# Kernel optimization log

Hardware: AMD Instinct MI355X
Metric: run time of the kernel (lower is better)

## Reference

```python
import jax, jax.numpy as jnp
import numpy as np

COORD_W, EDGE_W, COUNT_W, REG_W, CONTRA_W = 1.0, 2.0, 0.1, 0.001, 0.1
MARGIN = 1.0


def setup_inputs() -> dict:
    key = jax.random.key(0)
    ks = jax.random.split(key, 6)
    B, N, D, C = 16, 1024, 128, 2
    return {
        "predicted_coords": jax.random.normal(ks[0], (B, N, C), jnp.float32),
        "points": jax.random.normal(ks[1], (B, N, C), jnp.float32),
        "adjacency_logits": jax.random.normal(ks[2], (B, N, N), jnp.float32),
        "adjacency": jax.random.bernoulli(ks[3], 0.1, (B, N, N)).astype(jnp.float32),
        "node_masks": jnp.ones((B, N), jnp.float32),  # all nodes valid -> n_actual = N
        "predicted_count": jax.random.normal(ks[4], (B, 1), jnp.float32),
        "node_features": jax.random.normal(ks[5], (B, N, D), jnp.float32),
    }


def _bce_with_logits(logits, targets):
    # mean-reduced, numerically stable (matches F.binary_cross_entropy_with_logits)
    return jnp.mean(jnp.maximum(logits, 0.0) - logits * targets
                    + jnp.log1p(jnp.exp(-jnp.abs(logits))))


def _smooth_l1(pred, target):
    d = jnp.abs(pred - target)
    return jnp.mean(jnp.where(d < 1.0, 0.5 * d * d, d - 0.5))


def _contrastive_sample(features, adj):
    # features: [N, D], adj: [N, N]. torch.cdist pairwise euclidean via gram trick.
    nrm = jnp.sum(features * features, axis=-1)              # [N]
    sq = jnp.maximum(nrm[:, None] + nrm[None, :]
                     - 2.0 * (features @ features.T), 0.0)   # [N, N] squared dists
    n = features.shape[0]
    eye = jnp.eye(n, dtype=bool)
    pos_mask = adj > 0.5
    neg_mask = (adj <= 0.5) & (~eye)
    # positive term: mean of distances**2 over positive pairs == mean squared dist
    pos = jnp.sum(jnp.where(pos_mask, sq, 0.0)) / jnp.maximum(jnp.sum(pos_mask), 1)
    dist = jnp.sqrt(jnp.maximum(sq, 1e-12))
    hinge = jnp.square(jax.nn.relu(MARGIN - dist))
    neg = jnp.sum(jnp.where(neg_mask, hinge, 0.0)) / jnp.maximum(jnp.sum(neg_mask), 1)
    return pos + neg


def reference(predicted_coords, points, adjacency_logits, adjacency,
              node_masks, predicted_count, node_features):
    # node_masks are all ones, so the per-sample [:n_actual] slicing is the
    # full tensor; per-sample MSE/BCE means averaged over batch equal global means.
    coord_loss = jnp.mean(jnp.square(predicted_coords - points))
    edge_loss = _bce_with_logits(adjacency_logits, adjacency)
    actual_counts = jnp.sum(node_masks, axis=1)              # [B]
    count_loss = _smooth_l1(predicted_count[:, 0], actual_counts)
    reg_loss = jnp.mean(jnp.square(node_features))
    # contrastive path uses targets['adjacency'] (no predicted_adjacency key)
    contra_loss = jnp.mean(jax.vmap(_contrastive_sample)(node_features, adjacency))
    total = (COORD_W * coord_loss + EDGE_W * edge_loss + COUNT_W * count_loss
             + REG_W * reg_loss + CONTRA_W * contra_loss)
    return total, coord_loss, edge_loss, count_loss, reg_loss, contra_loss
```

## Files before the change

kernel.cpp:

```cpp
#include <hip/hip_runtime.h>
#include <hip/hip_bf16.h>

#define NN    1024
#define DD    128
#define TILE  128
#define PITCH 136
#define SQP   132
#define NBLK  1024

typedef __bf16 bf16_t;
typedef bf16_t bf16x8 __attribute__((ext_vector_type(8)));
typedef float  f32x4  __attribute__((ext_vector_type(4)));


__global__ __launch_bounds__(256) void small_losses(
    const float* __restrict__ pcoord, const float* __restrict__ pts,
    const float* __restrict__ masks,  const float* __restrict__ pcount,
    float* __restrict__ ws) {
  __shared__ float sh[4][2];
  float coord = 0.f, cnt = 0.f;

  const int gt = blockIdx.x * 256 + threadIdx.x;
  const int stride = 16 * 256;

  const float4* a4 = (const float4*)pcoord;
  const float4* b4 = (const float4*)pts;
  for (int i = gt; i < 8192; i += stride) {
    float4 a = a4[i], b = b4[i];
    float dx = a.x-b.x, dy = a.y-b.y, dz = a.z-b.z, dw = a.w-b.w;
    coord += dx*dx + dy*dy + dz*dz + dw*dw;
  }
  const float* m = masks + blockIdx.x * NN;
  for (int i = threadIdx.x; i < NN; i += 256) cnt += m[i];

  const int lane = threadIdx.x & 63, w = threadIdx.x >> 6;
  #pragma unroll
  for (int o = 32; o; o >>= 1) {
    coord += __shfl_xor(coord, o);
    cnt   += __shfl_xor(cnt, o);
  }
  if (lane == 0) { sh[w][0] = coord; sh[w][1] = cnt; }
  __syncthreads();
  if (threadIdx.x == 0) {
    float c = 0.f, n = 0.f;
    for (int i = 0; i < 4; ++i) { c += sh[i][0]; n += sh[i][1]; }
    atomicAdd(&ws[0], c);
    float d = fabsf(pcount[blockIdx.x] - n);
    float term = (d < 1.f) ? 0.5f * d * d : d - 0.5f;
    atomicAdd(&ws[2], term);
  }
}

__device__ __forceinline__ void loss_elem(float l, float a, float s, int grow, int gcol,
    float& bsum, float& poss, float& posc, float& negs, float& negc) {
  bsum += fmaxf(l, 0.f) - l * a + __logf(1.f + __expf(-fabsf(l)));
  if (a > 0.5f) {
    poss += s; posc += 1.f;
  } else if (grow != gcol) {
    negc += 1.f;
    if (s < 1.f) {
      float d = sqrtf(fmaxf(s, 1e-12f));
      float h = 1.f - d;
      negs += h * h;
    }
  }
}

__global__ __launch_bounds__(512, 4) void fused_gram_bce(
    const float* __restrict__ logits, const float* __restrict__ adj,
    const float* __restrict__ feat, float* __restrict__ ws) {
  __shared__ __align__(16) char smem[2 * TILE * PITCH * sizeof(bf16_t)];
  bf16_t* lsA = (bf16_t*)smem;
  bf16_t* lsB = (bf16_t*)(smem + TILE * PITCH * sizeof(bf16_t));
  float*  sqb = (float*)smem;
  __shared__ float nrmA[TILE], nrmB[TILE];
  __shared__ float red[8][6];

  const int bx  = blockIdx.x;
  const int b   = bx >> 6;
  const int tid = bx & 63;
  const int ti  = (tid >> 3) << 7;
  const int tj  = (tid & 7)  << 7;
  const bool diag = ((tid >> 3) == (tid & 7));

  const int t = threadIdx.x;
  const float* fb = feat + (size_t)b * NN * DD;

  float regsum = 0.f;
  #pragma unroll
  for (int it = 0; it < 8; ++it) {
    int cid  = it * 512 + t;
    int tile = cid >> 11;
    int sub  = cid & 2047;
    int row  = sub >> 4;
    int c8   = sub & 15;
    const float* src = fb + (size_t)((tile ? tj : ti) + row) * DD + c8 * 8;
    float4 u = *(const float4*)src;
    float4 v = *(const float4*)(src + 4);
    if (diag && tile == 0)
      regsum += u.x*u.x + u.y*u.y + u.z*u.z + u.w*u.w
              + v.x*v.x + v.y*v.y + v.z*v.z + v.w*v.w;
    bf16_t* dst = (tile ? lsB : lsA) + row * PITCH + c8 * 8;
    dst[0] = (bf16_t)u.x; dst[1] = (bf16_t)u.y; dst[2] = (bf16_t)u.z; dst[3] = (bf16_t)u.w;
    dst[4] = (bf16_t)v.x; dst[5] = (bf16_t)v.y; dst[6] = (bf16_t)v.z; dst[7] = (bf16_t)v.w;
  }
  __syncthreads();

  {
    int row  = t >> 1;
    int half = t & 1;
    const bf16_t* src = (row < TILE ? lsA + row * PITCH : lsB + (row - TILE) * PITCH)
                        + half * 64;
    float s = 0.f;
    #pragma unroll
    for (int c = 0; c < 8; ++c) {
      bf16x8 ch = *(const bf16x8*)(src + c * 8);
      #pragma unroll
      for (int i = 0; i < 8; ++i) { float v = (float)ch[i]; s += v * v; }
    }
    s += __shfl_xor(s, 1);
    if (half == 0) { if (row < TILE) nrmA[row] = s; else nrmB[row - TILE] = s; }
  }

  const int lane = t & 63;
  const int wave = t >> 6;
  const int lrow = lane & 15;
  const int quad = lane >> 4;

  f32x4 acc[8];
  #pragma unroll
  for (int fc = 0; fc < 8; ++fc) acc[fc] = (f32x4){0.f, 0.f, 0.f, 0.f};

  #pragma unroll
  for (int k0 = 0; k0 < DD; k0 += 32) {
    const int kc = k0 + quad * 8;
    bf16x8 aF = *(const bf16x8*)&lsA[(wave * 16 + lrow) * PITCH + kc];
    bf16x8 bF[8];
    #pragma unroll
    for (int fc = 0; fc < 8; ++fc)
      bF[fc] = *(const bf16x8*)&lsB[(fc * 16 + lrow) * PITCH + kc];
    #pragma unroll
    for (int fc = 0; fc < 8; ++fc)
      acc[fc] = __builtin_amdgcn_mfma_f32_16x16x32_bf16(aF, bF[fc], acc[fc], 0, 0, 0);
  }

  const int c4 = t & 31, r0 = t >> 5;
  const int gcol0 = tj + c4 * 4;
  const size_t base = (size_t)b * NN * NN;
  const float* lp = logits + base + (size_t)(ti + r0) * NN + gcol0;
  const float* ap = adj    + base + (size_t)(ti + r0) * NN + gcol0;
  float4 Lb[8], Ab[8];
  #pragma unroll
  for (int i = 0; i < 8; ++i) {
    Lb[i] = *(const float4*)(lp + (size_t)i * 16 * NN);
    Ab[i] = *(const float4*)(ap + (size_t)i * 16 * NN);
  }

  __syncthreads();

  {
    const int rbase = wave * 16 + quad * 4;
    #pragma unroll
    for (int fc = 0; fc < 8; ++fc) {
      const int ctile = fc * 16 + lrow;
      const float ncol = nrmB[ctile];
      #pragma unroll
      for (int r = 0; r < 4; ++r) {
        const int rtile = rbase + r;
        sqb[rtile * SQP + ctile] = fmaxf(nrmA[rtile] + ncol - 2.f * acc[fc][r], 0.f);
      }
    }
  }
  __syncthreads();

  float bsum = 0.f, poss = 0.f, posc = 0.f, negs = 0.f, negc = 0.f;
  #pragma unroll
  for (int it = 0; it < 8; ++it) {
    const int row  = it * 16 + r0;
    const int grow = ti + row;
    float4 L = Lb[it], A = Ab[it];
    float4 s = *(const float4*)&sqb[row * SQP + c4 * 4];
    loss_elem(L.x, A.x, s.x, grow, gcol0 + 0, bsum, poss, posc, negs, negc);
    loss_elem(L.y, A.y, s.y, grow, gcol0 + 1, bsum, poss, posc, negs, negc);
    loss_elem(L.z, A.z, s.z, grow, gcol0 + 2, bsum, poss, posc, negs, negc);
    loss_elem(L.w, A.w, s.w, grow, gcol0 + 3, bsum, poss, posc, negs, negc);
  }

  #pragma unroll
  for (int o = 32; o; o >>= 1) {
    bsum   += __shfl_xor(bsum, o);
    poss   += __shfl_xor(poss, o);
    posc   += __shfl_xor(posc, o);
    negs   += __shfl_xor(negs, o);
    negc   += __shfl_xor(negc, o);
    regsum += __shfl_xor(regsum, o);
  }
  if (lane == 0) {
    red[wave][0] = bsum; red[wave][1] = poss; red[wave][2] = posc;
    red[wave][3] = negs; red[wave][4] = negc; red[wave][5] = regsum;
  }
  __syncthreads();
  if (t == 0) {
    float s0=0.f,s1=0.f,s2=0.f,s3=0.f,s4=0.f,s5=0.f;
    for (int w = 0; w < 8; ++w) {
      s0 += red[w][0]; s1 += red[w][1]; s2 += red[w][2];
      s3 += red[w][3]; s4 += red[w][4]; s5 += red[w][5];
    }
    atomicAdd(&ws[3], s0);
    atomicAdd(&ws[4 + b], s1);
    atomicAdd(&ws[20 + b], s2);
    atomicAdd(&ws[36 + b], s3);
    atomicAdd(&ws[52 + b], s4);
    if (diag) atomicAdd(&ws[1], s5);
  }
}

__global__ void finalize(const float* __restrict__ ws, float* __restrict__ out) {
  if (threadIdx.x != 0 || blockIdx.x != 0) return;
  float coord = ws[0] / 32768.f;
  float reg   = ws[1] / 2097152.f;
  float cntl  = ws[2] / 16.f;
  float edge  = ws[3] / 16777216.f;
  float contra = 0.f;
  for (int b = 0; b < 16; ++b) {
    float p = ws[4 + b]  / fmaxf(ws[20 + b], 1.f);
    float n = ws[36 + b] / fmaxf(ws[52 + b], 1.f);
    contra += p + n;
  }
  contra *= (1.f / 16.f);
  float total = coord + 2.f * edge + 0.1f * cntl + 0.001f * reg + 0.1f * contra;
  out[0] = total; out[1] = coord; out[2] = edge;
  out[3] = cntl;  out[4] = reg;   out[5] = contra;
}

extern "C" void kernel_launch(void* const* d_in, const int* in_sizes, int n_in,
                              void* d_out, int out_size, void* d_ws, size_t ws_size,
                              hipStream_t stream) {
  (void)in_sizes; (void)n_in; (void)out_size; (void)ws_size;
  const float* pcoord = (const float*)d_in[0];
  const float* pts    = (const float*)d_in[1];
  const float* logits = (const float*)d_in[2];
  const float* adj    = (const float*)d_in[3];
  const float* masks  = (const float*)d_in[4];
  const float* pcount = (const float*)d_in[5];
  const float* nf     = (const float*)d_in[6];
  float* ws  = (float*)d_ws;
  float* out = (float*)d_out;

  hipMemsetAsync(ws, 0, 68 * sizeof(float), stream);
  small_losses<<<16, 256, 0, stream>>>(pcoord, pts, masks, pcount, ws);
  fused_gram_bce<<<NBLK, 512, 0, stream>>>(logits, adj, nf, ws);
  finalize<<<1, 64, 0, stream>>>(ws, out);
}
```

Before: 199.8 us.

## Split gram and BCE into separate kernels with fp16 distance buffer and prefetching

Splits the fused gram/BCE kernel into two kernels. The first computes squared pairwise distances via MFMA and writes them to an fp16 workspace buffer. The second streams logits, adjacency and the stored distances with a 4-deep register prefetch loop. This aims to improve memory-level parallelism over the fused kernel, whose loads were issued once behind barriers. In exchange it adds extra global traffic for the distance buffer and an extra launch, reduces distance precision to fp16, and needs a large workspace, falling back to the fused kernel otherwise.

New measurement: 268.2 us. +34.2%, slower.

```diff
diff --git a/kernel.cpp b/kernel.cpp
--- a/kernel.cpp
+++ b/kernel.cpp
@@ -11,6 +11,7 @@
 typedef __bf16 bf16_t;
 typedef bf16_t bf16x8 __attribute__((ext_vector_type(8)));
 typedef float  f32x4  __attribute__((ext_vector_type(4)));
+typedef _Float16 half4 __attribute__((ext_vector_type(4)));
 
 
 __global__ __launch_bounds__(256) void small_losses(
@@ -19,7 +20,6 @@
     float* __restrict__ ws) {
   __shared__ float sh[4][2];
   float coord = 0.f, cnt = 0.f;
-
   const int gt = blockIdx.x * 256 + threadIdx.x;
   const int stride = 16 * 256;
 
@@ -66,15 +66,15 @@
   }
 }
 
-__global__ __launch_bounds__(512, 4) void fused_gram_bce(
-    const float* __restrict__ logits, const float* __restrict__ adj,
-    const float* __restrict__ feat, float* __restrict__ ws) {
+__global__ __launch_bounds__(512, 4) void gram_sq(
+    const float* __restrict__ feat, _Float16* __restrict__ sqout,
+    float* __restrict__ ws) {
   __shared__ __align__(16) char smem[2 * TILE * PITCH * sizeof(bf16_t)];
   bf16_t* lsA = (bf16_t*)smem;
   bf16_t* lsB = (bf16_t*)(smem + TILE * PITCH * sizeof(bf16_t));
   float*  sqb = (float*)smem;
   __shared__ float nrmA[TILE], nrmB[TILE];
-  __shared__ float red[8][6];
+  __shared__ float red[8];
 
   const int bx  = blockIdx.x;
   const int b   = bx >> 6;
@@ -143,6 +143,193 @@
     for (int fc = 0; fc < 8; ++fc)
       acc[fc] = __builtin_amdgcn_mfma_f32_16x16x32_bf16(aF, bF[fc], acc[fc], 0, 0, 0);
   }
+  __syncthreads();
+
+  {
+    const int rbase = wave * 16 + quad * 4;
+    #pragma unroll
+    for (int fc = 0; fc < 8; ++fc) {
+      const int ctile = fc * 16 + lrow;
+      const float ncol = nrmB[ctile];
+      #pragma unroll
+      for (int r = 0; r < 4; ++r) {
+        const int rtile = rbase + r;
+        sqb[rtile * SQP + ctile] = fmaxf(nrmA[rtile] + ncol - 2.f * acc[fc][r], 0.f);
+      }
+    }
+  }
+  __syncthreads();
+
+  {
+    const int c4 = t & 31, r0 = t >> 5;
+    _Float16* sb = sqout + (size_t)b * NN * NN + (size_t)(ti + r0) * NN + tj + c4 * 4;
+    #pragma unroll
+    for (int it = 0; it < 8; ++it) {
+      float4 s = *(const float4*)&sqb[(it * 16 + r0) * SQP + c4 * 4];
+      half4 h = { (_Float16)s.x, (_Float16)s.y, (_Float16)s.z, (_Float16)s.w };
+      *(half4*)(sb + (size_t)it * 16 * NN) = h;
+    }
+  }
+
+  if (diag) {
+    #pragma unroll
+    for (int o = 32; o; o >>= 1) regsum += __shfl_xor(regsum, o);
+    if (lane == 0) red[wave] = regsum;
+    __syncthreads();
+    if (t == 0) {
+      float s = 0.f;
+      for (int w = 0; w < 8; ++w) s += red[w];
+      atomicAdd(&ws[1], s);
+    }
+  }
+}
+
+__global__ __launch_bounds__(256, 6) void bce_stream(
+    const float* __restrict__ logits, const float* __restrict__ adj,
+    const _Float16* __restrict__ sq, float* __restrict__ ws) {
+  __shared__ float red[4][5];
+  const int b   = blockIdx.x >> 6;
+  const int blk = blockIdx.x & 63;
+  const int t   = threadIdx.x;
+  const int row0 = blk * 16;
+  const int gcol0 = t * 4;
+
+  const size_t base = (size_t)b * NN * NN + (size_t)row0 * NN + gcol0;
+  const float*    lp = logits + base;
+  const float*    ap = adj + base;
+  const _Float16* sp = sq + base;
+
+  float4 Lb[4], Ab[4];
+  half4  Sb[4];
+  #pragma unroll
+  for (int i = 0; i < 4; ++i) {
+    Lb[i] = *(const float4*)(lp + (size_t)i * NN);
+    Ab[i] = *(const float4*)(ap + (size_t)i * NN);
+    Sb[i] = *(const half4*)(sp + (size_t)i * NN);
+  }
+
+  float bsum = 0.f, poss = 0.f, posc = 0.f, negs = 0.f, negc = 0.f;
+  #pragma unroll
+  for (int it = 0; it < 16; ++it) {
+    float4 L = Lb[it & 3], A = Ab[it & 3];
+    half4  S = Sb[it & 3];
+    if (it < 12) {
+      Lb[it & 3] = *(const float4*)(lp + (size_t)(it + 4) * NN);
+      Ab[it & 3] = *(const float4*)(ap + (size_t)(it + 4) * NN);
+      Sb[it & 3] = *(const half4*)(sp + (size_t)(it + 4) * NN);
+    }
+    const int grow = row0 + it;
+    loss_elem(L.x, A.x, (float)S[0], grow, gcol0 + 0, bsum, poss, posc, negs, negc);
+    loss_elem(L.y, A.y, (float)S[1], grow, gcol0 + 1, bsum, poss, posc, negs, negc);
+    loss_elem(L.z, A.z, (float)S[2], grow, gcol0 + 2, bsum, poss, posc, negs, negc);
+    loss_elem(L.w, A.w, (float)S[3], grow, gcol0 + 3, bsum, poss, posc, negs, negc);
+  }
+
+  const int lane = t & 63, wave = t >> 6;
+  #pragma unroll
+  for (int o = 32; o; o >>= 1) {
+    bsum += __shfl_xor(bsum, o);
+    poss += __shfl_xor(poss, o);
+    posc += __shfl_xor(posc, o);
+    negs += __shfl_xor(negs, o);
+    negc += __shfl_xor(negc, o);
+  }
+  if (lane == 0) {
+    red[wave][0] = bsum; red[wave][1] = poss; red[wave][2] = posc;
+    red[wave][3] = negs; red[wave][4] = negc;
+  }
+  __syncthreads();
+  if (t == 0) {
+    float s0=0.f,s1=0.f,s2=0.f,s3=0.f,s4=0.f;
+    for (int w = 0; w < 4; ++w) {
+      s0 += red[w][0]; s1 += red[w][1]; s2 += red[w][2];
+      s3 += red[w][3]; s4 += red[w][4];
+    }
+    atomicAdd(&ws[3], s0);
+    atomicAdd(&ws[4 + b], s1);
+    atomicAdd(&ws[20 + b], s2);
+    atomicAdd(&ws[36 + b], s3);
+    atomicAdd(&ws[52 + b], s4);
+  }
+}
+
+__global__ __launch_bounds__(512, 4) void fused_gram_bce(
+    const float* __restrict__ logits, const float* __restrict__ adj,
+    const float* __restrict__ feat, float* __restrict__ ws) {
+  __shared__ __align__(16) char smem[2 * TILE * PITCH * sizeof(bf16_t)];
+  bf16_t* lsA = (bf16_t*)smem;
+  bf16_t* lsB = (bf16_t*)(smem + TILE * PITCH * sizeof(bf16_t));
+  float*  sqb = (float*)smem;
+  __shared__ float nrmA[TILE], nrmB[TILE];
+  __shared__ float red[8][6];
+
+  const int bx  = blockIdx.x;
+  const int b   = bx >> 6;
+  const int tid = bx & 63;
+  const int ti  = (tid >> 3) << 7;
+  const int tj  = (tid & 7)  << 7;
+  const bool diag = ((tid >> 3) == (tid & 7));
+
+  const int t = threadIdx.x;
+  const float* fb = feat + (size_t)b * NN * DD;
+
+  float regsum = 0.f;
+  #pragma unroll
+  for (int it = 0; it < 8; ++it) {
+    int cid  = it * 512 + t;
+    int tile = cid >> 11;
+    int sub  = cid & 2047;
+    int row  = sub >> 4;
+    int c8   = sub & 15;
+    const float* src = fb + (size_t)((tile ? tj : ti) + row) * DD + c8 * 8;
+    float4 u = *(const float4*)src;
+    float4 v = *(const float4*)(src + 4);
+    if (diag && tile == 0)
+      regsum += u.x*u.x + u.y*u.y + u.z*u.z + u.w*u.w
+              + v.x*v.x + v.y*v.y + v.z*v.z + v.w*v.w;
+    bf16_t* dst = (tile ? lsB : lsA) + row * PITCH + c8 * 8;
+    dst[0] = (bf16_t)u.x; dst[1] = (bf16_t)u.y; dst[2] = (bf16_t)u.z; dst[3] = (bf16_t)u.w;
+    dst[4] = (bf16_t)v.x; dst[5] = (bf16_t)v.y; dst[6] = (bf16_t)v.z; dst[7] = (bf16_t)v.w;
+  }
+  __syncthreads();
+
+  {
+    int row  = t >> 1;
+    int half = t & 1;
+    const bf16_t* src = (row < TILE ? lsA + row * PITCH : lsB + (row - TILE) * PITCH)
+                        + half * 64;
+    float s = 0.f;
+    #pragma unroll
+    for (int c = 0; c < 8; ++c) {
+      bf16x8 ch = *(const bf16x8*)(src + c * 8);
+      #pragma unroll
+      for (int i = 0; i < 8; ++i) { float v = (float)ch[i]; s += v * v; }
+    }
+    s += __shfl_xor(s, 1);
+    if (half == 0) { if (row < TILE) nrmA[row] = s; else nrmB[row - TILE] = s; }
+  }
+
+  const int lane = t & 63;
+  const int wave = t >> 6;
+  const int lrow = lane & 15;
+  const int quad = lane >> 4;
+
+  f32x4 acc[8];
+  #pragma unroll
+  for (int fc = 0; fc < 8; ++fc) acc[fc] = (f32x4){0.f, 0.f, 0.f, 0.f};
+
+  #pragma unroll
+  for (int k0 = 0; k0 < DD; k0 += 32) {
+    const int kc = k0 + quad * 8;
+    bf16x8 aF = *(const bf16x8*)&lsA[(wave * 16 + lrow) * PITCH + kc];
+    bf16x8 bF[8];
+    #pragma unroll
+    for (int fc = 0; fc < 8; ++fc)
+      bF[fc] = *(const bf16x8*)&lsB[(fc * 16 + lrow) * PITCH + kc];
+    #pragma unroll
+    for (int fc = 0; fc < 8; ++fc)
+      acc[fc] = __builtin_amdgcn_mfma_f32_16x16x32_bf16(aF, bF[fc], acc[fc], 0, 0, 0);
+  }
 
   const int c4 = t & 31, r0 = t >> 5;
   const int gcol0 = tj + c4 * 4;
@@ -236,7 +423,7 @@
 extern "C" void kernel_launch(void* const* d_in, const int* in_sizes, int n_in,
                               void* d_out, int out_size, void* d_ws, size_t ws_size,
                               hipStream_t stream) {
-  (void)in_sizes; (void)n_in; (void)out_size; (void)ws_size;
+  (void)in_sizes; (void)n_in; (void)out_size;
   const float* pcoord = (const float*)d_in[0];
   const float* pts    = (const float*)d_in[1];
   const float* logits = (const float*)d_in[2];
@@ -247,8 +434,15 @@
   float* ws  = (float*)d_ws;
   float* out = (float*)d_out;
 
+  const size_t need = 1024 + (size_t)16 * NN * NN * 2;
   hipMemsetAsync(ws, 0, 68 * sizeof(float), stream);
   small_losses<<<16, 256, 0, stream>>>(pcoord, pts, masks, pcount, ws);
-  fused_gram_bce<<<NBLK, 512, 0, stream>>>(logits, adj, nf, ws);
+  if (ws_size >= need) {
+    _Float16* sqbuf = (_Float16*)((char*)d_ws + 1024);
+    gram_sq<<<NBLK, 512, 0, stream>>>(nf, sqbuf, ws);
+    bce_stream<<<1024, 256, 0, stream>>>(logits, adj, sqbuf, ws);
+  } else {
+    fused_gram_bce<<<NBLK, 512, 0, stream>>>(logits, adj, nf, ws);
+  }
   finalize<<<1, 64, 0, stream>>>(ws, out);
 }
```

## Split fused gram+BCE kernel into gram producer and streaming loss kernel

Applied to the files above, without the earlier changes.

Splits the fused kernel in two. The first computes squared pairwise distances with MFMA and writes them to workspace as fp16. The second streams logits, adjacency and the fp16 distances row-wise to accumulate the BCE and contrastive sums. The negative-pair count is now derived analytically in finalize instead of being counted. This decouples the compute-heavy gram stage from the bandwidth-bound stream, at the cost of an extra 32 MB fp16 write and read round trip, one more launch, and lower precision on the distances.

After: 226.6 us. 13.4% more time.

```diff
diff --git a/kernel.cpp b/kernel.cpp
--- a/kernel.cpp
+++ b/kernel.cpp
@@ -11,6 +11,7 @@
 typedef __bf16 bf16_t;
 typedef bf16_t bf16x8 __attribute__((ext_vector_type(8)));
 typedef float  f32x4  __attribute__((ext_vector_type(4)));
+typedef _Float16 half4 __attribute__((ext_vector_type(4)));
 
 
 __global__ __launch_bounds__(256) void small_losses(
@@ -19,7 +20,6 @@
     float* __restrict__ ws) {
   __shared__ float sh[4][2];
   float coord = 0.f, cnt = 0.f;
-
   const int gt = blockIdx.x * 256 + threadIdx.x;
   const int stride = 16 * 256;
 
@@ -51,30 +51,28 @@
   }
 }
 
-__device__ __forceinline__ void loss_elem(float l, float a, float s, int grow, int gcol,
-    float& bsum, float& poss, float& posc, float& negs, float& negc) {
+__device__ __forceinline__ void loss_elem(float l, float a, float s, bool offd,
+    float& bsum, float& poss, float& posc, float& negs) {
   bsum += fmaxf(l, 0.f) - l * a + __logf(1.f + __expf(-fabsf(l)));
-  if (a > 0.5f) {
-    poss += s; posc += 1.f;
-  } else if (grow != gcol) {
-    negc += 1.f;
-    if (s < 1.f) {
-      float d = sqrtf(fmaxf(s, 1e-12f));
-      float h = 1.f - d;
-      negs += h * h;
-    }
-  }
-}
-
-__global__ __launch_bounds__(512, 4) void fused_gram_bce(
-    const float* __restrict__ logits, const float* __restrict__ adj,
-    const float* __restrict__ feat, float* __restrict__ ws) {
+  const bool pos = a > 0.5f;
+  poss += pos ? s : 0.f;
+  posc += pos ? 1.f : 0.f;
+  if (!pos && offd && s < 1.f) {
+    float d = sqrtf(fmaxf(s, 1e-12f));
+    float h = 1.f - d;
+    negs += h * h;
+  }
+}
+
+__global__ __launch_bounds__(512, 4) void gram_sq(
+    const float* __restrict__ feat, _Float16* __restrict__ sqout,
+    float* __restrict__ ws) {
   __shared__ __align__(16) char smem[2 * TILE * PITCH * sizeof(bf16_t)];
   bf16_t* lsA = (bf16_t*)smem;
   bf16_t* lsB = (bf16_t*)(smem + TILE * PITCH * sizeof(bf16_t));
   float*  sqb = (float*)smem;
   __shared__ float nrmA[TILE], nrmB[TILE];
-  __shared__ float red[8][6];
+  __shared__ float red[8];
 
   const int bx  = blockIdx.x;
   const int b   = bx >> 6;
@@ -143,19 +141,6 @@
     for (int fc = 0; fc < 8; ++fc)
       acc[fc] = __builtin_amdgcn_mfma_f32_16x16x32_bf16(aF, bF[fc], acc[fc], 0, 0, 0);
   }
-
-  const int c4 = t & 31, r0 = t >> 5;
-  const int gcol0 = tj + c4 * 4;
-  const size_t base = (size_t)b * NN * NN;
-  const float* lp = logits + base + (size_t)(ti + r0) * NN + gcol0;
-  const float* ap = adj    + base + (size_t)(ti + r0) * NN + gcol0;
-  float4 Lb[8], Ab[8];
-  #pragma unroll
-  for (int i = 0; i < 8; ++i) {
-    Lb[i] = *(const float4*)(lp + (size_t)i * 16 * NN);
-    Ab[i] = *(const float4*)(ap + (size_t)i * 16 * NN);
-  }
-
   __syncthreads();
 
   {
@@ -173,45 +158,78 @@
   }
   __syncthreads();
 
-  float bsum = 0.f, poss = 0.f, posc = 0.f, negs = 0.f, negc = 0.f;
-  #pragma unroll
-  for (int it = 0; it < 8; ++it) {
-    const int row  = it * 16 + r0;
-    const int grow = ti + row;
-    float4 L = Lb[it], A = Ab[it];
-    float4 s = *(const float4*)&sqb[row * SQP + c4 * 4];
-    loss_elem(L.x, A.x, s.x, grow, gcol0 + 0, bsum, poss, posc, negs, negc);
-    loss_elem(L.y, A.y, s.y, grow, gcol0 + 1, bsum, poss, posc, negs, negc);
-    loss_elem(L.z, A.z, s.z, grow, gcol0 + 2, bsum, poss, posc, negs, negc);
-    loss_elem(L.w, A.w, s.w, grow, gcol0 + 3, bsum, poss, posc, negs, negc);
-  }
-
+  {
+    const int c4 = t & 31, r0 = t >> 5;
+    _Float16* sb = sqout + (size_t)b * NN * NN + (size_t)(ti + r0) * NN + tj + c4 * 4;
+    for (int it = 0; it < 8; ++it) {
+      float4 s = *(const float4*)&sqb[(it * 16 + r0) * SQP + c4 * 4];
+      half4 h = { (_Float16)s.x, (_Float16)s.y, (_Float16)s.z, (_Float16)s.w };
+      *(half4*)(sb + (size_t)it * 16 * NN) = h;
+    }
+  }
+
+  if (diag) {
+    #pragma unroll
+    for (int o = 32; o; o >>= 1) regsum += __shfl_xor(regsum, o);
+    if (lane == 0) red[wave] = regsum;
+    __syncthreads();
+    if (t == 0) {
+      float s = 0.f;
+      for (int w = 0; w < 8; ++w) s += red[w];
+      atomicAdd(&ws[1], s);
+    }
+  }
+}
+
+__global__ __launch_bounds__(256) void bce_stream(
+    const float* __restrict__ logits, const float* __restrict__ adj,
+    const _Float16* __restrict__ sq, float* __restrict__ ws) {
+  __shared__ float red[4][4];
+  const int b   = blockIdx.x >> 7;
+  const int blk = blockIdx.x & 127;
+  const int t   = threadIdx.x;
+  const int row0 = blk * 8;
+  const size_t base = (size_t)b * NN * NN + (size_t)row0 * NN;
+  const float4* lp = (const float4*)(logits + base);
+  const float4* ap = (const float4*)(adj + base);
+  const half4*  sp = (const half4*)(sq + base);
+
+  float bsum = 0.f, poss = 0.f, posc = 0.f, negs = 0.f;
+  #pragma unroll 2
+  for (int i = t; i < 2048; i += 256) {
+    float4 L = lp[i];
+    float4 A = ap[i];
+    half4  S = sp[i];
+    const int grow  = row0 + (i >> 8);
+    const int gcol0 = (i & 255) * 4;
+    loss_elem(L.x, A.x, (float)S[0], grow != gcol0 + 0, bsum, poss, posc, negs);
+    loss_elem(L.y, A.y, (float)S[1], grow != gcol0 + 1, bsum, poss, posc, negs);
+    loss_elem(L.z, A.z, (float)S[2], grow != gcol0 + 2, bsum, poss, posc, negs);
+    loss_elem(L.w, A.w, (float)S[3], grow != gcol0 + 3, bsum, poss, posc, negs);
+  }
+
+  const int lane = t & 63, wave = t >> 6;
   #pragma unroll
   for (int o = 32; o; o >>= 1) {
-    bsum   += __shfl_xor(bsum, o);
-    poss   += __shfl_xor(poss, o);
-    posc   += __shfl_xor(posc, o);
-    negs   += __shfl_xor(negs, o);
-    negc   += __shfl_xor(negc, o);
-    regsum += __shfl_xor(regsum, o);
+    bsum += __shfl_xor(bsum, o);
+    poss += __shfl_xor(poss, o);
+    posc += __shfl_xor(posc, o);
+    negs += __shfl_xor(negs, o);
   }
   if (lane == 0) {
-    red[wave][0] = bsum; red[wave][1] = poss; red[wave][2] = posc;
-    red[wave][3] = negs; red[wave][4] = negc; red[wave][5] = regsum;
+    red[wave][0] = bsum; red[wave][1] = poss;
+    red[wave][2] = posc; red[wave][3] = negs;
   }
   __syncthreads();
   if (t == 0) {
-    float s0=0.f,s1=0.f,s2=0.f,s3=0.f,s4=0.f,s5=0.f;
-    for (int w = 0; w < 8; ++w) {
-      s0 += red[w][0]; s1 += red[w][1]; s2 += red[w][2];
-      s3 += red[w][3]; s4 += red[w][4]; s5 += red[w][5];
+    float s0=0.f,s1=0.f,s2=0.f,s3=0.f;
+    for (int w = 0; w < 4; ++w) {
+      s0 += red[w][0]; s1 += red[w][1]; s2 += red[w][2]; s3 += red[w][3];
     }
     atomicAdd(&ws[3], s0);
     atomicAdd(&ws[4 + b], s1);
     atomicAdd(&ws[20 + b], s2);
     atomicAdd(&ws[36 + b], s3);
-    atomicAdd(&ws[52 + b], s4);
-    if (diag) atomicAdd(&ws[1], s5);
   }
 }
 
@@ -223,8 +241,9 @@
   float edge  = ws[3] / 16777216.f;
   float contra = 0.f;
   for (int b = 0; b < 16; ++b) {
+    float negcnt = 1048576.f - 1024.f - ws[20 + b];
     float p = ws[4 + b]  / fmaxf(ws[20 + b], 1.f);
-    float n = ws[36 + b] / fmaxf(ws[52 + b], 1.f);
+    float n = ws[36 + b] / fmaxf(negcnt, 1.f);
     contra += p + n;
   }
   contra *= (1.f / 16.f);
@@ -236,7 +255,7 @@
 extern "C" void kernel_launch(void* const* d_in, const int* in_sizes, int n_in,
                               void* d_out, int out_size, void* d_ws, size_t ws_size,
                               hipStream_t stream) {
-  (void)in_sizes; (void)n_in; (void)out_size; (void)ws_size;
+  (void)in_sizes; (void)n_in; (void)out_size;
   const float* pcoord = (const float*)d_in[0];
   const float* pts    = (const float*)d_in[1];
   const float* logits = (const float*)d_in[2];
@@ -249,6 +268,8 @@
 
   hipMemsetAsync(ws, 0, 68 * sizeof(float), stream);
   small_losses<<<16, 256, 0, stream>>>(pcoord, pts, masks, pcount, ws);
-  fused_gram_bce<<<NBLK, 512, 0, stream>>>(logits, adj, nf, ws);
+  _Float16* sqbuf = (_Float16*)((char*)d_ws + 1024);
+  gram_sq<<<NBLK, 512, 0, stream>>>(nf, sqbuf, ws);
+  bce_stream<<<2048, 256, 0, stream>>>(logits, adj, sqbuf, ws);
   finalize<<<1, 64, 0, stream>>>(ws, out);
 }
```
